# Kernel optimization log

Hardware: AMD Instinct MI355X
Metric: run time of the kernel (lower is better)

The kernel has to match this reference:

```python
import jax, jax.numpy as jnp
import numpy as np

B, T, E = 64, 2048, 1024

def setup_inputs() -> dict:
    key = jax.random.key(0)
    k1, k2, k3, k4 = jax.random.split(key, 4)
    x = jax.random.normal(k1, (B, T, E), dtype=jnp.float32)
    c = jax.random.normal(k2, (B, E), dtype=jnp.float32)
    W = jax.random.normal(k3, (E, 1), dtype=jnp.float32) * 0.05
    b = jnp.zeros((T, 1), dtype=jnp.float32)
    U = jax.random.normal(k4, (E, T), dtype=jnp.float32) * 0.05
    return {"x": x, "c": c, "W": W, "b": b, "U": U}

def reference(x, c, W, b, U):
    # et: (B,T) = c @ U + squeeze(x @ W + b, -1)
    et = jnp.einsum('be,et->bt', c, U) + (jnp.einsum('bte,eo->bto', x, W) + b)[..., 0]
    at = jax.nn.softmax(et, axis=-1)                 # (B,T)
    # weighted sum over timesteps -> (B,E)
    return jnp.einsum('bt,bte->be', at, x)
```

## Files before the change

### kernel.cpp

```cpp
#include <hip/hip_runtime.h>
#include <stdint.h>

#define BB 64
#define TT 2048
#define EE 1024
#define ST 32
#define TBLK (TT / ST)
#define BG 2
#define NBG (BB / BG)
#define RPP 4
#define NPH (BG * TBLK / RPP)

#define S_OFF 0
#define O_OFF 2048

#define PHASE(ph, CUR, NXT)                                                    \
  do {                                                                         \
    if ((ph) + 1 < NPH) {                                                      \
      const int bl1 = ((ph) + 1) >> 4, tl1 = (((ph) + 1) & 15) * RPP;          \
      const float4* srcp = xq + ((size_t)bl1 * TT + tl1) * 256;                \
      _Pragma("unroll")                                                        \
      for (int r = 0; r < 4; ++r) NXT[r] = srcp[(size_t)r * 256];              \
    }                                                                          \
    float s_[4];                                                               \
    _Pragma("unroll")                                                          \
    for (int r = 0; r < 4; ++r)                                                \
      s_[r] = CUR[r].x * wf.x + CUR[r].y * wf.y +                              \
              CUR[r].z * wf.z + CUR[r].w * wf.w;                               \
                        \
    float t_[2];                                                               \
    _Pragma("unroll")                                                          \
    for (int r = 0; r < 2; ++r) {                                              \
      const float ar = s_[r]     + __shfl_xor(s_[r],     32, 64);              \
      const float br = s_[r + 2] + __shfl_xor(s_[r + 2], 32, 64);              \
      t_[r] = (lane < 32) ? ar : br;                                           \
    }                                                                          \
                                 \
    float u_;                                                                  \
    {                                                                          \
      const float ar = t_[0] + __shfl_xor(t_[0], 16, 64);                      \
      const float br = t_[1] + __shfl_xor(t_[1], 16, 64);                      \
      u_ = ((lane & 16) == 0) ? ar : br;                                       \
    }                                                                          \
    u_ += __shfl_xor(u_, 8, 64);                                               \
    u_ += __shfl_xor(u_, 4, 64);                                               \
    u_ += __shfl_xor(u_, 2, 64);                                               \
    u_ += __shfl_xor(u_, 1, 64);                                               \
    if ((lane & 15) == 0) ex[(ph) & 1][lane >> 4][wu] = u_;                    \
    asm volatile("s_waitcnt lgkmcnt(0)" ::: "memory");                         \
    __builtin_amdgcn_s_barrier();                                              \
    asm volatile("" ::: "memory");                                             \
    const int bl_ = (ph) >> 4, tl_ = ((ph) & 15) * RPP;                        \
    const float4 cu4 = *(const float4*)&cu_s[bl_][tl_];                        \
    float et[4];                                                               \
    _Pragma("unroll")                                                          \
    for (int r = 0; r < 4; ++r) {                                              \
      const float4 q = ((const float4*)ex[(ph) & 1])[r];   \
      et[r] = (q.x + q.y) + (q.z + q.w);                                       \
    }                                                                          \
    et[0] += cu4.x; et[1] += cu4.y; et[2] += cu4.z; et[3] += cu4.w;            \
    float p_[4];                                                               \
    _Pragma("unroll")                                                          \
    for (int r = 0; r < 4; ++r) p_[r] = __expf(et[r]);                         \
    l += (p_[0] + p_[1]) + (p_[2] + p_[3]);                                    \
    _Pragma("unroll")                                                          \
    for (int r = 0; r < 4; ++r) {                                              \
      o.x = fmaf(p_[r], CUR[r].x, o.x); o.y = fmaf(p_[r], CUR[r].y, o.y);      \
      o.z = fmaf(p_[r], CUR[r].z, o.z); o.w = fmaf(p_[r], CUR[r].w, o.w);      \
    }                                                                          \
    if (((ph) & 15) == 15) {                                                   \
      const int pi = (b0 + bl_) * ST + ts;                                     \
      ((float4*)O_part)[(size_t)pi * 256 + (wu << 6) + lane] = o;              \
      if (tid == 0) S_part[pi] = l;                                            \
      l = 0.f; o = make_float4(0.f, 0.f, 0.f, 0.f);                            \
    }                                                                          \
  } while (0)

__global__ __launch_bounds__(256, 4) void k_fused(
    const float* __restrict__ x, const float* __restrict__ c,
    const float* __restrict__ W, const float* __restrict__ bvec,
    const float* __restrict__ U,
    float* __restrict__ S_part, float* __restrict__ O_part)
{
    const int bg   = blockIdx.x >> 5;
    const int ts   = blockIdx.x & 31;
    const int b0   = bg * BG;
    const int t0   = ts * TBLK;
    const int tid  = threadIdx.x;
    const int wu   = __builtin_amdgcn_readfirstlane(tid >> 6);
    const int lane = tid & 63;

    __shared__ float cu_s[BG][TBLK];
    __shared__ float pcu[4][BG][TBLK];
    __shared__ float ex[2][4][4];

    const float4* xq = (const float4*)x + ((size_t)b0 * TT + t0) * 256 + (wu << 6) + lane;

    float4 XA[4], XB[4];
    #pragma unroll
    for (int r = 0; r < 4; ++r) XA[r] = xq[(size_t)r * 256];

    {
        const float* cb = c + (size_t)b0 * EE + (wu << 8);
        const float* Ub = U + ((size_t)(wu << 8)) * TT + t0 + lane;
        float a0 = 0.f, a1 = 0.f;
        #pragma unroll 8
        for (int e = 0; e < 256; ++e) {
            const float u = Ub[(size_t)e * TT];
            a0 = fmaf(cb[e], u, a0);
            a1 = fmaf(cb[EE + e], u, a1);
        }
        pcu[wu][0][lane] = a0;
        pcu[wu][1][lane] = a1;
    }
    __syncthreads();
    if (tid < BG * TBLK) {
        const int j = tid >> 6, t = tid & 63;
        cu_s[j][t] = bvec[t0 + t] + pcu[0][j][t] + pcu[1][j][t] + pcu[2][j][t] + pcu[3][j][t];
    }
    __syncthreads();

    const float4 wf = ((const float4*)W)[(wu << 6) + lane];
    float  l = 0.f;
    float4 o = make_float4(0.f, 0.f, 0.f, 0.f);

    for (int ph = 0; ph < NPH; ph += 2) {
        PHASE(ph,     XA, XB);
        PHASE(ph + 1, XB, XA);
    }
}

__global__ __launch_bounds__(256) void k_merge(const float* __restrict__ S_part,
                                               const float* __restrict__ O_part,
                                               float* __restrict__ out) {
    const int b  = blockIdx.x >> 2;
    const int eq = blockIdx.x & 3;
    const int e  = eq * 256 + threadIdx.x;

    float S = 0.f, acc = 0.f;
    #pragma unroll 4
    for (int p = 0; p < ST; ++p) {
        const int pi = b * ST + p;
        S   += S_part[pi];
        acc += O_part[(size_t)pi * EE + e];
    }
    out[(size_t)b * EE + e] = acc / S;
}

extern "C" void kernel_launch(void* const* d_in, const int* in_sizes, int n_in,
                              void* d_out, int out_size, void* d_ws, size_t ws_size,
                              hipStream_t stream) {
    const float* x    = (const float*)d_in[0];
    const float* c    = (const float*)d_in[1];
    const float* W    = (const float*)d_in[2];
    const float* bvec = (const float*)d_in[3];
    const float* U    = (const float*)d_in[4];
    float* out = (float*)d_out;

    float* ws     = (float*)d_ws;
    float* S_part = ws + S_OFF;
    float* O_part = ws + O_OFF;

    k_fused<<<NBG * ST, 256, 0, stream>>>(x, c, W, bvec, U, S_part, O_part);
    k_merge<<<BB * 4, 256, 0, stream>>>(S_part, O_part, out);
}
```

Measured before the change: 126.2 us.

## Split c@U into its own kernel and give each wave an independent row segment

Moves the c@U + b projection into a separate kernel that writes a (B,T) buffer. The main kernel now assigns each wavefront its own 32-row segment of one batch, with the full E=1024 row in registers. Scores are reduced within the wave, so the per-phase LDS exchange and block barriers disappear. This costs an extra launch, a round trip of the cu buffer through global memory, twice as many partials for the merge kernel to read, and more registers per thread.

```diff
diff --git a/kernel.cpp b/kernel.cpp
--- a/kernel.cpp
+++ b/kernel.cpp
@@ -4,130 +4,121 @@
 #define BB 64
 #define TT 2048
 #define EE 1024
-#define ST 32
-#define TBLK (TT / ST)
-#define BG 2
-#define NBG (BB / BG)
-#define RPP 4
-#define NPH (BG * TBLK / RPP)
+#define SEGS 64
+#define RWS 32
+#define NBT 16
 
-#define S_OFF 0
-#define O_OFF 2048
+#define CU_OFF 0
+#define S_OFF  (BB * TT)
+#define O_OFF  (S_OFF + BB * SEGS)
 
-#define PHASE(ph, CUR, NXT)                                                    \
+#define CUQC(i) ((i) % 4 == 0 ? cuq[(i) / 4].x : \
+                ((i) % 4 == 1 ? cuq[(i) / 4].y : \
+                ((i) % 4 == 2 ? cuq[(i) / 4].z : cuq[(i) / 4].w)))
+
+#define BATCH(bt, CUR, NXT)                                                    \
   do {                                                                         \
-    if ((ph) + 1 < NPH) {                                                      \
-      const int bl1 = ((ph) + 1) >> 4, tl1 = (((ph) + 1) & 15) * RPP;          \
-      const float4* srcp = xq + ((size_t)bl1 * TT + tl1) * 256;                \
+    if ((bt) + 1 < NBT) {                                                      \
+      const float4* np = xw + (size_t)((bt) + 1) * 2 * 256;                    \
       _Pragma("unroll")                                                        \
-      for (int r = 0; r < 4; ++r) NXT[r] = srcp[(size_t)r * 256];              \
+      for (int k = 0; k < 4; ++k) NXT[k] = np[64 * k];                         \
+      _Pragma("unroll")                                                        \
+      for (int k = 0; k < 4; ++k) NXT[4 + k] = np[256 + 64 * k];               \
     }                                                                          \
-    float s_[4];                                                               \
+    float s0 = 0.f, s1 = 0.f;                                                  \
     _Pragma("unroll")                                                          \
-    for (int r = 0; r < 4; ++r)                                                \
-      s_[r] = CUR[r].x * wf.x + CUR[r].y * wf.y +                              \
-              CUR[r].z * wf.z + CUR[r].w * wf.w;                               \
-                        \
-    float t_[2];                                                               \
+    for (int k = 0; k < 4; ++k) {                                              \
+      s0 += CUR[k].x * wf[k].x + CUR[k].y * wf[k].y +                          \
+            CUR[k].z * wf[k].z + CUR[k].w * wf[k].w;                           \
+      s1 += CUR[4 + k].x * wf[k].x + CUR[4 + k].y * wf[k].y +                  \
+            CUR[4 + k].z * wf[k].z + CUR[4 + k].w * wf[k].w;                   \
+    }                                                                          \
     _Pragma("unroll")                                                          \
-    for (int r = 0; r < 2; ++r) {                                              \
-      const float ar = s_[r]     + __shfl_xor(s_[r],     32, 64);              \
-      const float br = s_[r + 2] + __shfl_xor(s_[r + 2], 32, 64);              \
-      t_[r] = (lane < 32) ? ar : br;                                           \
+    for (int off = 32; off >= 1; off >>= 1) {                                  \
+      s0 += __shfl_xor(s0, off, 64);                                           \
+      s1 += __shfl_xor(s1, off, 64);                                           \
     }                                                                          \
-                                 \
-    float u_;                                                                  \
-    {                                                                          \
-      const float ar = t_[0] + __shfl_xor(t_[0], 16, 64);                      \
-      const float br = t_[1] + __shfl_xor(t_[1], 16, 64);                      \
-      u_ = ((lane & 16) == 0) ? ar : br;                                       \
-    }                                                                          \
-    u_ += __shfl_xor(u_, 8, 64);                                               \
-    u_ += __shfl_xor(u_, 4, 64);                                               \
-    u_ += __shfl_xor(u_, 2, 64);                                               \
-    u_ += __shfl_xor(u_, 1, 64);                                               \
-    if ((lane & 15) == 0) ex[(ph) & 1][lane >> 4][wu] = u_;                    \
-    asm volatile("s_waitcnt lgkmcnt(0)" ::: "memory");                         \
-    __builtin_amdgcn_s_barrier();                                              \
-    asm volatile("" ::: "memory");                                             \
-    const int bl_ = (ph) >> 4, tl_ = ((ph) & 15) * RPP;                        \
-    const float4 cu4 = *(const float4*)&cu_s[bl_][tl_];                        \
-    float et[4];                                                               \
+    const float et0 = s0 + CUQC(2 * (bt));                                     \
+    const float et1 = s1 + CUQC(2 * (bt) + 1);                                 \
+    const float p0 = __expf(et0), p1 = __expf(et1);                            \
+    l += p0 + p1;                                                              \
     _Pragma("unroll")                                                          \
-    for (int r = 0; r < 4; ++r) {                                              \
-      const float4 q = ((const float4*)ex[(ph) & 1])[r];   \
-      et[r] = (q.x + q.y) + (q.z + q.w);                                       \
-    }                                                                          \
-    et[0] += cu4.x; et[1] += cu4.y; et[2] += cu4.z; et[3] += cu4.w;            \
-    float p_[4];                                                               \
-    _Pragma("unroll")                                                          \
-    for (int r = 0; r < 4; ++r) p_[r] = __expf(et[r]);                         \
-    l += (p_[0] + p_[1]) + (p_[2] + p_[3]);                                    \
-    _Pragma("unroll")                                                          \
-    for (int r = 0; r < 4; ++r) {                                              \
-      o.x = fmaf(p_[r], CUR[r].x, o.x); o.y = fmaf(p_[r], CUR[r].y, o.y);      \
-      o.z = fmaf(p_[r], CUR[r].z, o.z); o.w = fmaf(p_[r], CUR[r].w, o.w);      \
-    }                                                                          \
-    if (((ph) & 15) == 15) {                                                   \
-      const int pi = (b0 + bl_) * ST + ts;                                     \
-      ((float4*)O_part)[(size_t)pi * 256 + (wu << 6) + lane] = o;              \
-      if (tid == 0) S_part[pi] = l;                                            \
-      l = 0.f; o = make_float4(0.f, 0.f, 0.f, 0.f);                            \
+    for (int k = 0; k < 4; ++k) {                                              \
+      o[k].x += p0 * CUR[k].x + p1 * CUR[4 + k].x;                             \
+      o[k].y += p0 * CUR[k].y + p1 * CUR[4 + k].y;                             \
+      o[k].z += p0 * CUR[k].z + p1 * CUR[4 + k].z;                             \
+      o[k].w += p0 * CUR[k].w + p1 * CUR[4 + k].w;                             \
     }                                                                          \
   } while (0)
 
-__global__ __launch_bounds__(256, 4) void k_fused(
-    const float* __restrict__ x, const float* __restrict__ c,
-    const float* __restrict__ W, const float* __restrict__ bvec,
-    const float* __restrict__ U,
+__global__ __launch_bounds__(256) void k_cu(const float* __restrict__ c,
+                                            const float* __restrict__ bvec,
+                                            const float* __restrict__ U,
+                                            float* __restrict__ cu) {
+    const int tch = blockIdx.x & 7;
+    const int b   = blockIdx.x >> 3;
+    const int t   = tch * 256 + threadIdx.x;
+
+    const float* cb = c + (size_t)b * EE;
+    const float* Up = U + t;
+    float a0 = 0.f, a1 = 0.f, a2 = 0.f, a3 = 0.f;
+    #pragma unroll 4
+    for (int e = 0; e < EE; e += 4) {
+        a0 = fmaf(cb[e + 0], Up[(size_t)(e + 0) * TT], a0);
+        a1 = fmaf(cb[e + 1], Up[(size_t)(e + 1) * TT], a1);
+        a2 = fmaf(cb[e + 2], Up[(size_t)(e + 2) * TT], a2);
+        a3 = fmaf(cb[e + 3], Up[(size_t)(e + 3) * TT], a3);
+    }
+    cu[(size_t)b * TT + t] = bvec[t] + (a0 + a1) + (a2 + a3);
+}
+
+__global__ __launch_bounds__(256, 3) void k_fused(
+    const float* __restrict__ x, const float* __restrict__ cu,
+    const float* __restrict__ W,
     float* __restrict__ S_part, float* __restrict__ O_part)
 {
-    const int bg   = blockIdx.x >> 5;
-    const int ts   = blockIdx.x & 31;
-    const int b0   = bg * BG;
-    const int t0   = ts * TBLK;
     const int tid  = threadIdx.x;
     const int wu   = __builtin_amdgcn_readfirstlane(tid >> 6);
     const int lane = tid & 63;
+    const int wid  = blockIdx.x * 4 + wu;
+    const int b    = wid >> 6;
+    const int seg  = wid & 63;
 
-    __shared__ float cu_s[BG][TBLK];
-    __shared__ float pcu[4][BG][TBLK];
-    __shared__ float ex[2][4][4];
+    const size_t row0 = (size_t)b * TT + seg * RWS;
+    const float4* xw  = (const float4*)x + row0 * 256 + lane;
 
-    const float4* xq = (const float4*)x + ((size_t)b0 * TT + t0) * 256 + (wu << 6) + lane;
+    float4 XA[8], XB[8];
+    #pragma unroll
+    for (int k = 0; k < 4; ++k) XA[k] = xw[64 * k];
+    #pragma unroll
+    for (int k = 0; k < 4; ++k) XA[4 + k] = xw[256 + 64 * k];
 
-    float4 XA[4], XB[4];
+    float4 wf[4];
     #pragma unroll
-    for (int r = 0; r < 4; ++r) XA[r] = xq[(size_t)r * 256];
+    for (int k = 0; k < 4; ++k) wf[k] = ((const float4*)W)[lane + 64 * k];
 
+    float4 cuq[8];
     {
-        const float* cb = c + (size_t)b0 * EE + (wu << 8);
-        const float* Ub = U + ((size_t)(wu << 8)) * TT + t0 + lane;
-        float a0 = 0.f, a1 = 0.f;
-        #pragma unroll 8
-        for (int e = 0; e < 256; ++e) {
-            const float u = Ub[(size_t)e * TT];
-            a0 = fmaf(cb[e], u, a0);
-            a1 = fmaf(cb[EE + e], u, a1);
-        }
-        pcu[wu][0][lane] = a0;
-        pcu[wu][1][lane] = a1;
+        const float4* cup = (const float4*)(cu + row0);
+        #pragma unroll
+        for (int i = 0; i < 8; ++i) cuq[i] = cup[i];
     }
-    __syncthreads();
-    if (tid < BG * TBLK) {
-        const int j = tid >> 6, t = tid & 63;
-        cu_s[j][t] = bvec[t0 + t] + pcu[0][j][t] + pcu[1][j][t] + pcu[2][j][t] + pcu[3][j][t];
+
+    float  l = 0.f;
+    float4 o[4];
+    #pragma unroll
+    for (int k = 0; k < 4; ++k) o[k] = make_float4(0.f, 0.f, 0.f, 0.f);
+
+    #pragma unroll
+    for (int bt = 0; bt < NBT; bt += 2) {
+        BATCH(bt,     XA, XB);
+        BATCH(bt + 1, XB, XA);
     }
-    __syncthreads();
 
-    const float4 wf = ((const float4*)W)[(wu << 6) + lane];
-    float  l = 0.f;
-    float4 o = make_float4(0.f, 0.f, 0.f, 0.f);
-
-    for (int ph = 0; ph < NPH; ph += 2) {
-        PHASE(ph,     XA, XB);
-        PHASE(ph + 1, XB, XA);
-    }
+    #pragma unroll
+    for (int k = 0; k < 4; ++k)
+        ((float4*)O_part)[(size_t)wid * 256 + lane + 64 * k] = o[k];
+    if (lane == 0) S_part[wid] = l;
 }
 
 __global__ __launch_bounds__(256) void k_merge(const float* __restrict__ S_part,
@@ -139,8 +130,8 @@
 
     float S = 0.f, acc = 0.f;
     #pragma unroll 4
-    for (int p = 0; p < ST; ++p) {
-        const int pi = b * ST + p;
+    for (int p = 0; p < SEGS; ++p) {
+        const int pi = b * SEGS + p;
         S   += S_part[pi];
         acc += O_part[(size_t)pi * EE + e];
     }
@@ -158,9 +149,11 @@
     float* out = (float*)d_out;
 
     float* ws     = (float*)d_ws;
+    float* cu     = ws + CU_OFF;
     float* S_part = ws + S_OFF;
     float* O_part = ws + O_OFF;
 
-    k_fused<<<NBG * ST, 256, 0, stream>>>(x, c, W, bvec, U, S_part, O_part);
+    k_cu<<<BB * 8, 256, 0, stream>>>(c, bvec, U, cu);
+    k_fused<<<(BB * SEGS) / 4, 256, 0, stream>>>(x, cu, W, S_part, O_part);
     k_merge<<<BB * 4, 256, 0, stream>>>(S_part, O_part, out);
 }
```

Result: slower. 334.5 us (+165.0%).
